# Performance work log

Hardware: AMD Instinct MI355X
Metric: run time of the kernel (lower is better)

## Reference

```python
import jax, jax.numpy as jnp
import numpy as np

B, T, N = 8, 100, 100000
MARGIN = 0.1
THRESHOLD = 0.5
BIG = 1.0e9


def setup_inputs() -> dict:
    key = jax.random.key(0)
    k0, k1, k2, k3, k4 = jax.random.split(key, 5)
    outputs = jax.random.normal(k0, (B, T, 3), dtype=jnp.float32)
    c2ws = jax.random.normal(k1, (B, 4, 4), dtype=jnp.float32)
    scene_scales = jax.random.uniform(k2, (B,), dtype=jnp.float32)
    means = jax.random.normal(k3, (N, 3), dtype=jnp.float32)
    scales = jax.random.uniform(k4, (N, 3), dtype=jnp.float32)
    return {"outputs": outputs, "c2ws": c2ws, "scene_scales": scene_scales,
            "means": means, "scales": scales}


def reference(outputs, c2ws, scene_scales, means, scales):
    # per-splat max radius (precomputed in torch __init__)
    maxsplatrad = jnp.max(scales, axis=1)                      # [N]
    # world transform: aff = R * scene_scale, trans = translation
    aff = c2ws[:, :3, :3] * scene_scales[:, None, None]        # [B,3,3]
    trans = c2ws[:, :3, 3]                                     # [B,3]
    # baddbmm(trans, outputs, aff.mT) == outputs @ aff^T + trans
    retrajs = jnp.einsum('btd,bed->bte', outputs, aff) + trans[:, None, :]  # [B,T,3]
    # axis-aligned bbox of each trajectory, expanded by threshold
    thres = THRESHOLD * scene_scales[0]
    uvals = jnp.max(retrajs, axis=1) + thres                   # [B,3]
    lvals = jnp.min(retrajs, axis=1) - thres                   # [B,3]
    # bbox filter: which splats fall inside each trajectory bbox
    inside = jnp.all((means[None, :, :] >= lvals[:, None, :]) &
                     (means[None, :, :] <= uvals[:, None, :]), axis=2)  # [B,N]
    # pairwise distances via ||a-b||^2 = |a|^2 + |b|^2 - 2 a.b (avoids [B,T,N,3])
    r2 = jnp.sum(retrajs * retrajs, axis=-1)                   # [B,T]
    m2 = jnp.sum(means * means, axis=-1)                       # [N]
    cross = jnp.einsum('btd,nd->btn', retrajs, means)          # [B,T,N]
    d2 = r2[:, :, None] + m2[None, None, :] - 2.0 * cross
    dist = jnp.sqrt(jnp.maximum(d2, 0.0))
    resdists = dist - maxsplatrad[None, None, :] - MARGIN      # [B,T,N]
    # scatter_reduce amin with include_self=False and 1e9 default ==
    # masked min over splats; pairs not inside bbox never scattered -> BIG
    masked = jnp.where(inside[:, None, :], resdists, BIG)
    collosses = jnp.min(masked, axis=2)                        # [B,T]
    return jnp.sum(jax.nn.relu(-collosses)) / (B * T)
```

## Files before the change

### kernel.cpp

```cpp
#include <hip/hip_runtime.h>

constexpr int   B_ = 8;
constexpr int   T_ = 100;
constexpr int   NPAIRS = B_ * T_;
constexpr int   N_ = 100000;
constexpr float MARGIN_ = 0.1f;
constexpr float THRESHOLD_ = 0.5f;
constexpr float BIG_ = 1000000000.0f;

constexpr int PER   = 98;
constexpr int NBLK  = 1024;
constexpr int NSLOT = 1024;
constexpr int KCH   = 16;
constexpr int NRED  = NBLK / KCH;

constexpr size_t RES_OFF    = 0;
constexpr size_t SLOT_OFF   = RES_OFF + (size_t)NBLK * NSLOT * 4;
constexpr size_t BOUNDS_OFF = SLOT_OFF + (size_t)NSLOT * 16;
constexpr size_t KEYS_OFF   = BOUNDS_OFF + 256;
constexpr size_t CNT_OFF    = KEYS_OFF + (size_t)NSLOT * 4;

__device__ __forceinline__ float fsqrt(float x) { return __builtin_amdgcn_sqrtf(x); }

__device__ __forceinline__ unsigned fkey(float f) {
    unsigned u = __float_as_uint(f);
    return (u & 0x80000000u) ? ~u : (u | 0x80000000u);
}

__global__ void k_prep(const float* __restrict__ outputs,
                       const float* __restrict__ c2ws,
                       const float* __restrict__ ss,
                       char* ws) {
    __shared__ float re_s[NPAIRS * 3];
    int tid = threadIdx.x;
    float* bounds = (float*)(ws + BOUNDS_OFF);

    ((unsigned*)(ws + KEYS_OFF))[tid] = fkey(BIG_);
    if (tid == 0) *(unsigned*)(ws + CNT_OFF) = 0;

    if (tid < NPAIRS) {
        int b = tid / T_;
        float s = ss[b];
        const float* o = outputs + tid * 3;
        float o0 = o[0], o1 = o[1], o2 = o[2];
        const float* c = c2ws + b * 16;
#pragma unroll
        for (int e = 0; e < 3; e++) {
            re_s[tid * 3 + e] =
                (o0 * c[e * 4 + 0] + o1 * c[e * 4 + 1] + o2 * c[e * 4 + 2]) * s + c[e * 4 + 3];
        }
    }
    __syncthreads();

    if (tid < 24) {
        int b = tid / 3, e = tid - b * 3;
        float mx = -3.4e38f, mn = 3.4e38f;
        for (int t = 0; t < T_; t++) {
            float v = re_s[(b * T_ + t) * 3 + e];
            mx = fmaxf(mx, v);
            mn = fminf(mn, v);
        }
        float thres = THRESHOLD_ * ss[0];
        bounds[b * 3 + e]      = mn - thres;
        bounds[24 + b * 3 + e] = mx + thres;
    }

    int bb = tid >> 7, r = tid & 127;
    float4 q = make_float4(0.f, 0.f, 0.f, 0.f);
    if (r < T_) {
        int p = bb * T_ + r;
        q = make_float4(re_s[p * 3 + 0], re_s[p * 3 + 1], re_s[p * 3 + 2], 1.f);
    }
    ((float4*)(ws + SLOT_OFF))[tid] = q;
}

__global__ __launch_bounds__(256) void k_main(const float* __restrict__ means,
                                              const float* __restrict__ scales,
                                              const char* __restrict__ wsc,
                                              char* __restrict__ ws) {
    __shared__ float4 rec_s[PER * 3];
    int tid = threadIdx.x;
    const float4* sp     = (const float4*)(wsc + SLOT_OFF);
    const float*  bounds = (const float*)(wsc + BOUNDS_OFF);

    float4 q0 = sp[tid];
    float4 q1 = sp[tid + 256];
    float4 q2 = sp[tid + 512];
    float4 q3 = sp[tid + 768];

    if (tid < PER) {
        int n = blockIdx.x * PER + tid;
        float mx = 0.f, my = 0.f, mz = 0.f;
        float e0, e1, e2, e3, e4, e5, e6, e7;
        if (n < N_) {
            mx = means[(size_t)n * 3 + 0];
            my = means[(size_t)n * 3 + 1];
            mz = means[(size_t)n * 3 + 2];
            float msr = fmaxf(fmaxf(scales[(size_t)n * 3 + 0], scales[(size_t)n * 3 + 1]),
                              scales[(size_t)n * 3 + 2]) + MARGIN_;
            float e[8];
#pragma unroll
            for (int b = 0; b < 8; b++) {
                bool in = (mx >= bounds[b * 3 + 0]) & (mx <= bounds[24 + b * 3 + 0]) &
                          (my >= bounds[b * 3 + 1]) & (my <= bounds[24 + b * 3 + 1]) &
                          (mz >= bounds[b * 3 + 2]) & (mz <= bounds[24 + b * 3 + 2]);
                e[b] = in ? msr : -BIG_;
            }
            e0 = e[0]; e1 = e[1]; e2 = e[2]; e3 = e[3];
            e4 = e[4]; e5 = e[5]; e6 = e[6]; e7 = e[7];
        } else {
            e0 = e1 = e2 = e3 = e4 = e5 = e6 = e7 = -BIG_;
        }
        rec_s[tid * 3 + 0] = make_float4(mx, my, mz, 0.f);
        rec_s[tid * 3 + 1] = make_float4(e0, e2, e4, e6);
        rec_s[tid * 3 + 2] = make_float4(e1, e3, e5, e7);
    }
    __syncthreads();

    int effidx = 1 + ((__builtin_amdgcn_readfirstlane(tid) >> 7) & 1);

    float mn0 = BIG_, mn1 = BIG_, mn2 = BIG_, mn3 = BIG_;
#pragma unroll 2
    for (int i = 0; i < PER; i++) {
        float4 pos = rec_s[i * 3];
        float4 ef  = rec_s[i * 3 + effidx];
        float dx, dy, dz, d2;
        dx = q0.x - pos.x; dy = q0.y - pos.y; dz = q0.z - pos.z;
        d2 = fmaf(dz, dz, fmaf(dy, dy, dx * dx));
        mn0 = fminf(mn0, fsqrt(d2) - ef.x);
        dx = q1.x - pos.x; dy = q1.y - pos.y; dz = q1.z - pos.z;
        d2 = fmaf(dz, dz, fmaf(dy, dy, dx * dx));
        mn1 = fminf(mn1, fsqrt(d2) - ef.y);
        dx = q2.x - pos.x; dy = q2.y - pos.y; dz = q2.z - pos.z;
        d2 = fmaf(dz, dz, fmaf(dy, dy, dx * dx));
        mn2 = fminf(mn2, fsqrt(d2) - ef.z);
        dx = q3.x - pos.x; dy = q3.y - pos.y; dz = q3.z - pos.z;
        d2 = fmaf(dz, dz, fmaf(dy, dy, dx * dx));
        mn3 = fminf(mn3, fsqrt(d2) - ef.w);
    }

    float* res = (float*)(ws + RES_OFF) + (size_t)blockIdx.x * NSLOT;
    res[tid]       = mn0;
    res[tid + 256] = mn1;
    res[tid + 512] = mn2;
    res[tid + 768] = mn3;
}

__global__ __launch_bounds__(256) void k_red(const char* __restrict__ wsc,
                                             char* __restrict__ ws,
                                             float* __restrict__ out) {
    __shared__ int   isLast;
    __shared__ float wsum[4];
    int tid = threadIdx.x;
    const float* res  = (const float*)(wsc + RES_OFF);
    unsigned*    keys = (unsigned*)(ws + KEYS_OFF);
    unsigned*    cnt  = (unsigned*)(ws + CNT_OFF);

    const float* row = res + (size_t)blockIdx.x * KCH * NSLOT;
    float mn0 = BIG_, mn1 = BIG_, mn2 = BIG_, mn3 = BIG_;
#pragma unroll
    for (int i = 0; i < KCH; i++) {
        mn0 = fminf(mn0, row[tid]);
        mn1 = fminf(mn1, row[tid + 256]);
        mn2 = fminf(mn2, row[tid + 512]);
        mn3 = fminf(mn3, row[tid + 768]);
        row += NSLOT;
    }
    atomicMin(&keys[tid],       fkey(mn0));
    atomicMin(&keys[tid + 256], fkey(mn1));
    atomicMin(&keys[tid + 512], fkey(mn2));
    atomicMin(&keys[tid + 768], fkey(mn3));

    __threadfence();
    if (tid == 0) isLast = (atomicAdd(cnt, 1u) == (unsigned)(NRED - 1));
    __syncthreads();
    if (isLast) {
        __threadfence();
        float acc = 0.f;
        for (int s = tid; s < NSLOT; s += 256) {
            if ((s & 127) < T_) {
                unsigned k = __hip_atomic_load(&keys[s], __ATOMIC_RELAXED, __HIP_MEMORY_SCOPE_AGENT);
                unsigned u = (k & 0x80000000u) ? (k ^ 0x80000000u) : ~k;
                acc += fmaxf(0.f, -__uint_as_float(u));
            }
        }
#pragma unroll
        for (int off = 32; off; off >>= 1) acc += __shfl_down(acc, off, 64);
        if ((tid & 63) == 0) wsum[tid >> 6] = acc;
        __syncthreads();
        if (tid == 0)
            out[0] = (wsum[0] + wsum[1] + wsum[2] + wsum[3]) * (1.0f / (float)NPAIRS);
    }
}

extern "C" void kernel_launch(void* const* d_in, const int* in_sizes, int n_in,
                              void* d_out, int out_size, void* d_ws, size_t ws_size,
                              hipStream_t stream) {
    const float* outputs = (const float*)d_in[0];
    const float* c2ws    = (const float*)d_in[1];
    const float* ss      = (const float*)d_in[2];
    const float* means   = (const float*)d_in[3];
    const float* scales  = (const float*)d_in[4];
    float* out = (float*)d_out;
    char*  ws  = (char*)d_ws;

    hipLaunchKernelGGL(k_prep, dim3(1), dim3(1024), 0, stream, outputs, c2ws, ss, ws);
    hipLaunchKernelGGL(k_main, dim3(NBLK), dim3(256), 0, stream,
                       means, scales, (const char*)ws, ws);
    hipLaunchKernelGGL(k_red, dim3(NRED), dim3(256), 0, stream, (const char*)ws, ws, out);
}
```

Before: 98.70 us.

## Fuse prep kernel into main kernel by recomputing trajectories per block

Removes the single-block prep kernel and has every main block recompute the transformed trajectories and bbox bounds in shared memory. Block 0 also initializes the reduction keys and counter. This drops one kernel launch and the serial one-block prep stage. In exchange each of the 1024 blocks does redundant prep work (800 point transforms and a 24-thread 100-step min/max scan) before its main loop, and it uses more shared memory.

```diff
diff --git a/kernel.cpp b/kernel.cpp
--- a/kernel.cpp
+++ b/kernel.cpp
@@ -14,11 +14,9 @@
 constexpr int KCH   = 16;
 constexpr int NRED  = NBLK / KCH;
 
-constexpr size_t RES_OFF    = 0;
-constexpr size_t SLOT_OFF   = RES_OFF + (size_t)NBLK * NSLOT * 4;
-constexpr size_t BOUNDS_OFF = SLOT_OFF + (size_t)NSLOT * 16;
-constexpr size_t KEYS_OFF   = BOUNDS_OFF + 256;
-constexpr size_t CNT_OFF    = KEYS_OFF + (size_t)NSLOT * 4;
+constexpr size_t RES_OFF  = 0;
+constexpr size_t KEYS_OFF = RES_OFF + (size_t)NBLK * NSLOT * 4;
+constexpr size_t CNT_OFF  = KEYS_OFF + (size_t)NSLOT * 4;
 
 __device__ __forceinline__ float fsqrt(float x) { return __builtin_amdgcn_sqrtf(x); }
 
@@ -27,26 +25,35 @@
     return (u & 0x80000000u) ? ~u : (u | 0x80000000u);
 }
 
-__global__ void k_prep(const float* __restrict__ outputs,
-                       const float* __restrict__ c2ws,
-                       const float* __restrict__ ss,
-                       char* ws) {
-    __shared__ float re_s[NPAIRS * 3];
+__global__ __launch_bounds__(256) void k_main(const float* __restrict__ outputs,
+                                              const float* __restrict__ c2ws,
+                                              const float* __restrict__ ss,
+                                              const float* __restrict__ means,
+                                              const float* __restrict__ scales,
+                                              char* __restrict__ ws) {
+    __shared__ float  re_s[NPAIRS * 3];
+    __shared__ float  bounds_s[48];
+    __shared__ float4 rec_s[PER * 3];
     int tid = threadIdx.x;
-    float* bounds = (float*)(ws + BOUNDS_OFF);
-
-    ((unsigned*)(ws + KEYS_OFF))[tid] = fkey(BIG_);
-    if (tid == 0) *(unsigned*)(ws + CNT_OFF) = 0;
-
-    if (tid < NPAIRS) {
-        int b = tid / T_;
+
+    if (blockIdx.x == 0) {
+        unsigned* keys = (unsigned*)(ws + KEYS_OFF);
+        keys[tid]       = fkey(BIG_);
+        keys[tid + 256] = fkey(BIG_);
+        keys[tid + 512] = fkey(BIG_);
+        keys[tid + 768] = fkey(BIG_);
+        if (tid == 0) *(unsigned*)(ws + CNT_OFF) = 0;
+    }
+
+    for (int p = tid; p < NPAIRS; p += 256) {
+        int b = p / T_;
         float s = ss[b];
-        const float* o = outputs + tid * 3;
+        const float* o = outputs + p * 3;
         float o0 = o[0], o1 = o[1], o2 = o[2];
         const float* c = c2ws + b * 16;
 #pragma unroll
         for (int e = 0; e < 3; e++) {
-            re_s[tid * 3 + e] =
+            re_s[p * 3 + e] =
                 (o0 * c[e * 4 + 0] + o1 * c[e * 4 + 1] + o2 * c[e * 4 + 2]) * s + c[e * 4 + 3];
         }
     }
@@ -61,33 +68,26 @@
             mn = fminf(mn, v);
         }
         float thres = THRESHOLD_ * ss[0];
-        bounds[b * 3 + e]      = mn - thres;
-        bounds[24 + b * 3 + e] = mx + thres;
-    }
-
-    int bb = tid >> 7, r = tid & 127;
-    float4 q = make_float4(0.f, 0.f, 0.f, 0.f);
-    if (r < T_) {
-        int p = bb * T_ + r;
-        q = make_float4(re_s[p * 3 + 0], re_s[p * 3 + 1], re_s[p * 3 + 2], 1.f);
-    }
-    ((float4*)(ws + SLOT_OFF))[tid] = q;
-}
-
-__global__ __launch_bounds__(256) void k_main(const float* __restrict__ means,
-                                              const float* __restrict__ scales,
-                                              const char* __restrict__ wsc,
-                                              char* __restrict__ ws) {
-    __shared__ float4 rec_s[PER * 3];
-    int tid = threadIdx.x;
-    const float4* sp     = (const float4*)(wsc + SLOT_OFF);
-    const float*  bounds = (const float*)(wsc + BOUNDS_OFF);
-
-    float4 q0 = sp[tid];
-    float4 q1 = sp[tid + 256];
-    float4 q2 = sp[tid + 512];
-    float4 q3 = sp[tid + 768];
-
+        bounds_s[b * 3 + e]      = mn - thres;
+        bounds_s[24 + b * 3 + e] = mx + thres;
+    }
+    __syncthreads();
+
+    float4 q0, q1, q2, q3;
+    {
+        float4* qs[4] = {&q0, &q1, &q2, &q3};
+#pragma unroll
+        for (int j = 0; j < 4; j++) {
+            int g = tid + j * 256;
+            int bb = g >> 7, r = g & 127;
+            float4 q = make_float4(0.f, 0.f, 0.f, 0.f);
+            if (r < T_) {
+                int p = bb * T_ + r;
+                q = make_float4(re_s[p * 3 + 0], re_s[p * 3 + 1], re_s[p * 3 + 2], 0.f);
+            }
+            *qs[j] = q;
+        }
+    }
     if (tid < PER) {
         int n = blockIdx.x * PER + tid;
         float mx = 0.f, my = 0.f, mz = 0.f;
@@ -101,9 +101,9 @@
             float e[8];
 #pragma unroll
             for (int b = 0; b < 8; b++) {
-                bool in = (mx >= bounds[b * 3 + 0]) & (mx <= bounds[24 + b * 3 + 0]) &
-                          (my >= bounds[b * 3 + 1]) & (my <= bounds[24 + b * 3 + 1]) &
-                          (mz >= bounds[b * 3 + 2]) & (mz <= bounds[24 + b * 3 + 2]);
+                bool in = (mx >= bounds_s[b * 3 + 0]) & (mx <= bounds_s[24 + b * 3 + 0]) &
+                          (my >= bounds_s[b * 3 + 1]) & (my <= bounds_s[24 + b * 3 + 1]) &
+                          (mz >= bounds_s[b * 3 + 2]) & (mz <= bounds_s[24 + b * 3 + 2]);
                 e[b] = in ? msr : -BIG_;
             }
             e0 = e[0]; e1 = e[1]; e2 = e[2]; e3 = e[3];
@@ -204,8 +204,7 @@
     float* out = (float*)d_out;
     char*  ws  = (char*)d_ws;
 
-    hipLaunchKernelGGL(k_prep, dim3(1), dim3(1024), 0, stream, outputs, c2ws, ss, ws);
     hipLaunchKernelGGL(k_main, dim3(NBLK), dim3(256), 0, stream,
-                       means, scales, (const char*)ws, ws);
+                       outputs, c2ws, ss, means, scales, ws);
     hipLaunchKernelGGL(k_red, dim3(NRED), dim3(256), 0, stream, (const char*)ws, ws, out);
 }
```

After: 96.78 us. Within noise of the previous version (-2.0%).
